# Performance work log

Hardware: AMD Instinct MI355X
Metric: run time of the kernel (lower is better)

The kernel has to match this reference:

```python
import jax
import jax.numpy as jnp
from jax import lax
import numpy as np

INPUT_DIM = 784
HIDDEN_DIM = 1024
BATCH = 256
N_BINS = 10


def setup_inputs() -> dict:
    key = jax.random.key(0)
    k1, k2, k3, k4, k5 = jax.random.split(key, 5)
    # kaiming-normal-ish init scales (faithful in spirit; exact values irrelevant for math)
    W = jax.random.normal(k1, (HIDDEN_DIM, INPUT_DIM), dtype=jnp.float32) * np.sqrt(2.0 / INPUT_DIM)
    c = jnp.zeros((HIDDEN_DIM, 1), dtype=jnp.float32)
    V = jax.random.normal(k2, (INPUT_DIM, HIDDEN_DIM, N_BINS), dtype=jnp.float32) * np.sqrt(2.0 / N_BINS)
    b = jnp.zeros((INPUT_DIM, N_BINS), dtype=jnp.float32)
    x = jax.random.randint(k3, (BATCH, INPUT_DIM), 0, N_BINS, dtype=jnp.int32)
    return {"x": x, "W": W, "c": c, "V": V, "b": b}


def reference(x, W, c, V, b):
    # x: [B, D] int pixel bins; W: [H, D]; c: [H, 1]; V: [D, H, 10]; b: [D, 10]
    B = x.shape[0]
    xf = x.astype(jnp.float32)  # [B, D]
    a0 = jnp.broadcast_to(c[:, 0][None, :], (B, W.shape[0]))  # [B, H]

    def step(a, inp):
        Vi, bi, Wi, xi = inp  # Vi:[H,10], bi:[10], Wi:[H], xi:[B]
        h = jax.nn.sigmoid(a)                       # [B, H]
        p = jax.nn.softmax(h @ Vi + bi, axis=1)     # [B, 10]
        a = a + xi[:, None] * Wi[None, :]           # rank-1 update, matches x_i @ W[:,i].T
        return a, p

    _, p_seq = lax.scan(step, a0, (V, b, W.T, xf.T))  # p_seq: [D, B, 10]
    p_hat = jnp.transpose(p_seq, (1, 2, 0))            # [B, 10, D] == torch.stack(p_hat, dim=2)
    return p_hat
```

## Files before the change

kernel.cpp:

```cpp
#include <hip/hip_runtime.h>
#include <stdint.h>

#define D_DIM 784
#define H_DIM 1024
#define B_DIM 256
#define NBIN  10
#define G_CH  8
#define T_CH  98
#define BT    16
#define BF    2
#define LOG2E 1.4426950408889634f

#define PSCAN_BLKS 512
#define VPREP_BLKS D_DIM
#define WPREP_BLKS 208

typedef _Float16 half8_t  __attribute__((ext_vector_type(8)));
typedef __fp16   fp16x2_t __attribute__((ext_vector_type(2)));
typedef float    float4_t __attribute__((ext_vector_type(4)));

__global__ void k_prep2(const float* __restrict__ W, const float* __restrict__ V,
                        const float* __restrict__ c, const int* __restrict__ x,
                        _Float16* __restrict__ Wt2h, _Float16* __restrict__ VB,
                        _Float16* __restrict__ PA) {
    __shared__ __align__(16) float smem[H_DIM * NBIN];
    int tid = threadIdx.x;
    int bx  = blockIdx.x;

    if (bx < PSCAN_BLKS) {
        int q  = bx;
        int b0 = (q & 127) * BF;
        int h  = (q >> 7) * 256 + tid;
        float* xs0 = smem;
        float* xs1 = smem + D_DIM;
        for (int qq = tid; qq < BF * (D_DIM / 4); qq += 256) {
            int bb = qq / (D_DIM / 4), r = qq % (D_DIM / 4);
            int4 xi = ((const int4*)(x + (size_t)(b0 + bb) * D_DIM))[r];
            float4 xf = make_float4((float)xi.x, (float)xi.y, (float)xi.z, (float)xi.w);
            *((float4*)((bb ? xs1 : xs0) + r * 4)) = xf;
        }
        float acc0 = c[h], acc1 = acc0;
        __syncthreads();
        const float4* w4 = (const float4*)(W + (size_t)h * D_DIM);
        _Float16* pa = PA + (size_t)b0 * H_DIM + h;

        auto pstore = [&](int t_) {
            pa[(size_t)t_ * (B_DIM * H_DIM)]         = (_Float16)(acc0 * LOG2E);
            pa[(size_t)t_ * (B_DIM * H_DIM) + H_DIM] = (_Float16)(acc1 * LOG2E);
        };
        auto pfma = [&](float4 w0_, float4 w1_, int t_) {
            float4 xa0 = *((const float4*)(xs0 + t_ * 8));
            float4 xa1 = *((const float4*)(xs0 + t_ * 8 + 4));
            float4 xb0 = *((const float4*)(xs1 + t_ * 8));
            float4 xb1 = *((const float4*)(xs1 + t_ * 8 + 4));
            acc0 += xa0.x*w0_.x + xa0.y*w0_.y + xa0.z*w0_.z + xa0.w*w0_.w
                  + xa1.x*w1_.x + xa1.y*w1_.y + xa1.z*w1_.z + xa1.w*w1_.w;
            acc1 += xb0.x*w0_.x + xb0.y*w0_.y + xb0.z*w0_.z + xb0.w*w0_.w
                  + xb1.x*w1_.x + xb1.y*w1_.y + xb1.z*w1_.z + xb1.w*w1_.w;
        };

        float4 wA0 = w4[0], wA1 = w4[1], wB0 = w4[2], wB1 = w4[3];
        for (int t = 0; t < T_CH - 2; t += 2) {
            float4 nA0 = w4[(t + 2) * 2], nA1 = w4[(t + 2) * 2 + 1];
            float4 nB0 = w4[(t + 3) * 2], nB1 = w4[(t + 3) * 2 + 1];
            pstore(t);     pfma(wA0, wA1, t);
            pstore(t + 1); pfma(wB0, wB1, t + 1);
            wA0 = nA0; wA1 = nA1; wB0 = nB0; wB1 = nB1;
        }
        pstore(96); pfma(wA0, wA1, 96);
        pstore(97);
    } else if (bx < PSCAN_BLKS + VPREP_BLKS) {
        int i = bx - PSCAN_BLKS;
        const float4* src = (const float4*)(V + (size_t)i * H_DIM * NBIN);
        #pragma unroll
        for (int qv = 0; qv < 10; ++qv) {
            float4 v = src[qv * 256 + tid];
            *((float4*)&smem[(qv * 256 + tid) * 4]) = v;
        }
        __syncthreads();
        #pragma unroll
        for (int qv = 0; qv < 8; ++qv) {
            int pair = qv * 256 + tid;
            int kk = pair >> 6, ll = pair & 63;
            int n = ll & 15, hb = kk * 32 + ((ll >> 4) & 3) * 8;
            union { _Float16 hh[8]; uint4 u; } o;
            #pragma unroll
            for (int jj = 0; jj < 8; ++jj)
                o.hh[jj] = (_Float16)((n < NBIN) ? smem[(hb + jj) * NBIN + n] : 0.0f);
            ((uint4*)VB)[(size_t)i * 2048 + pair] = o.u;
        }
    } else {
        int qw = bx - PSCAN_BLKS - VPREP_BLKS;
        int j0 = (qw % 13) * 64, h0 = (qw / 13) * 64;
        float (*t)[65] = (float(*)[65])smem;
        int tj = tid & 63, tr = tid >> 6;
        int j = j0 + tj;
        #pragma unroll
        for (int r = 0; r < 16; ++r) {
            int hh = tr * 16 + r;
            t[hh][tj] = (j < D_DIM) ? W[(size_t)(h0 + hh) * D_DIM + j] : 0.0f;
        }
        __syncthreads();
        #pragma unroll
        for (int r = 0; r < 16; ++r) {
            int jj = tr * 16 + r;
            int jo = j0 + jj;
            if (jo < D_DIM) Wt2h[(size_t)jo * H_DIM + h0 + tj] = (_Float16)(t[tj][jj] * LOG2E);
        }
    }
}

__global__ __launch_bounds__(256, 4)
void k_main(const _Float16* __restrict__ VB, const _Float16* __restrict__ Wt2h,
            const _Float16* __restrict__ PA, const int* __restrict__ x,
            const float* __restrict__ bias, float* __restrict__ out) {
    int bt  = blockIdx.x;
    int tc  = blockIdx.y;
    int tid = threadIdx.x;
    int w   = tid >> 6;
    int l   = tid & 63;
    int bl  = l & 15;
    int kg  = l >> 4;
    int bg  = bt * BT + bl;
    int i0  = tc * G_CH;

    __shared__ __align__(16) _Float16 wlds[G_CH][H_DIM];
    __shared__ float red[4][64][18];
    __shared__ float bs[G_CH][16];

    {
        int ii = tid >> 4, n = tid & 15;
        if (ii < G_CH) bs[ii][n] = (n < NBIN) ? bias[(size_t)(i0 + ii) * NBIN + n] : 0.0f;
    }
    {
        #pragma unroll
        for (int r = 0; r < G_CH; ++r) {
            uint2 v = ((const uint2*)(Wt2h + (size_t)(i0 + r) * H_DIM))[tid];
            *((uint2*)&wlds[r][tid * 4]) = v;
        }
    }
    float xvf[G_CH];
    {
        const int4* xp = (const int4*)(x + (size_t)bg * D_DIM + i0);
        int4 x0 = xp[0], x1 = xp[1];
        xvf[0] = (float)x0.x; xvf[1] = (float)x0.y; xvf[2] = (float)x0.z; xvf[3] = (float)x0.w;
        xvf[4] = (float)x1.x; xvf[5] = (float)x1.y; xvf[6] = (float)x1.z; xvf[7] = (float)x1.w;
    }
    float a[8][8];
    {
        const _Float16* src = PA + ((size_t)tc * B_DIM + bg) * H_DIM + w * 256 + kg * 8;
        #pragma unroll
        for (int m = 0; m < 8; ++m) {
            half8_t av = *((const half8_t*)(src + m * 32));
            #pragma unroll
            for (int j = 0; j < 8; ++j) a[m][j] = (float)av[j];
        }
    }

    const uint4* vp = (const uint4*)VB + ((size_t)i0 * 32 + w * 8) * 64 + l;
    uint4 vbuf[3];
    vbuf[0] = vp[0];
    vbuf[1] = vp[64];
    float4_t acc = {0.f, 0.f, 0.f, 0.f};

    auto step = [&](int mm) {
        const int ii = mm >> 3, m = mm & 7;
        if (mm + 2 < 64) {
            const int nn = mm + 2;
            vbuf[nn % 3] = vp[((nn >> 3) * 32 + (nn & 7)) * 64];
        }
        union { half8_t h8; uint u32[4]; } af;
        #pragma unroll
        for (int p = 0; p < 4; ++p) {
            float s0 = __builtin_amdgcn_rcpf(1.0f + __builtin_amdgcn_exp2f(-a[m][2 * p]));
            float s1 = __builtin_amdgcn_rcpf(1.0f + __builtin_amdgcn_exp2f(-a[m][2 * p + 1]));
            union { fp16x2_t v; uint u; } cv;
            cv.v = __builtin_amdgcn_cvt_pkrtz(s0, s1);
            af.u32[p] = cv.u;
        }
        union { half8_t h8; uint4 u; } bf;
        bf.u = vbuf[mm % 3];
        acc = __builtin_amdgcn_mfma_f32_16x16x32_f16(af.h8, bf.h8, acc, 0, 0, 0);
        half8_t wh = *((const half8_t*)&wlds[ii][w * 256 + kg * 8 + m * 32]);
        float xf = xvf[ii];
        a[m][0] += xf * (float)wh[0]; a[m][1] += xf * (float)wh[1];
        a[m][2] += xf * (float)wh[2]; a[m][3] += xf * (float)wh[3];
        a[m][4] += xf * (float)wh[4]; a[m][5] += xf * (float)wh[5];
        a[m][6] += xf * (float)wh[6]; a[m][7] += xf * (float)wh[7];
        if (m == 7) {
            int s = (ii & 3) * 4;
            red[w][l][s + 0] = acc[0]; red[w][l][s + 1] = acc[1];
            red[w][l][s + 2] = acc[2]; red[w][l][s + 3] = acc[3];
            acc = (float4_t){0.f, 0.f, 0.f, 0.f};
        }
    };

    auto softmax_store = [&](int half) {
        float p4[4];
        #pragma unroll
        for (int q = 0; q < 4; ++q) {
            int ii = half * 4 + q;
            float tot = red[0][l][q * 4 + w] + red[1][l][q * 4 + w]
                      + red[2][l][q * 4 + w] + red[3][l][q * 4 + w];
            float v = (bl < NBIN) ? tot + bs[ii][bl] : -3.0e38f;
            float vm = v;
            vm = fmaxf(vm, __shfl_xor(vm, 1));
            vm = fmaxf(vm, __shfl_xor(vm, 2));
            vm = fmaxf(vm, __shfl_xor(vm, 4));
            vm = fmaxf(vm, __shfl_xor(vm, 8));
            float e = __builtin_amdgcn_exp2f((v - vm) * LOG2E);
            float ss = e;
            ss += __shfl_xor(ss, 1); ss += __shfl_xor(ss, 2);
            ss += __shfl_xor(ss, 4); ss += __shfl_xor(ss, 8);
            p4[q] = e * __builtin_amdgcn_rcpf(ss);
        }
        if (bl < NBIN) {
            int b = bt * BT + kg * 4 + w;
            size_t base = ((size_t)b * NBIN + bl) * D_DIM + i0 + half * 4;
            float4 v = make_float4(p4[0], p4[1], p4[2], p4[3]);
            *((float4*)(out + base)) = v;
        }
    };

    __syncthreads();
    #pragma unroll
    for (int mm = 0; mm < 32; ++mm) step(mm);
    __syncthreads();
    softmax_store(0);
    __syncthreads();
    #pragma unroll
    for (int mm = 32; mm < 64; ++mm) step(mm);
    __syncthreads();
    softmax_store(1);
}

extern "C" void kernel_launch(void* const* d_in, const int* in_sizes, int n_in,
                              void* d_out, int out_size, void* d_ws, size_t ws_size,
                              hipStream_t stream) {
    const int*   x    = (const int*)d_in[0];
    const float* W    = (const float*)d_in[1];
    const float* c    = (const float*)d_in[2];
    const float* V    = (const float*)d_in[3];
    const float* bias = (const float*)d_in[4];
    float* out = (float*)d_out;

    char* ws = (char*)d_ws;
    size_t off = 0;
    _Float16* Wt2h = (_Float16*)(ws + off);
    off += (size_t)D_DIM * H_DIM * sizeof(_Float16);
    off = (off + 255) & ~(size_t)255;
    _Float16* VB = (_Float16*)(ws + off);
    off += (size_t)D_DIM * 32 * 64 * 8 * sizeof(_Float16);
    off = (off + 255) & ~(size_t)255;
    _Float16* PA = (_Float16*)(ws + off);

    k_prep2<<<dim3(PSCAN_BLKS + VPREP_BLKS + WPREP_BLKS), 256, 0, stream>>>(W, V, c, x, Wt2h, VB, PA);
    k_main<<<dim3(B_DIM / BT, T_CH), 256, 0, stream>>>(VB, Wt2h, PA, x, bias, out);
}
```

Before: 218.9 us.

## Halve prep LDS footprint and register-block prefix scan over two hidden units

The prefix-sum part of the prep kernel now has each thread handle two adjacent hidden units, which halves the number of scan blocks, reuses each shared x load across four accumulators, and writes packed half2 stores. The V-repack branch now processes its slice in two halves so shared memory shrinks from 40KB to 20KB, aiming for more resident blocks per CU. The cost is an extra barrier in the V path, more registers per thread in the scan, and fewer scan blocks to spread across the GPU.

```diff
diff --git a/kernel.cpp b/kernel.cpp
--- a/kernel.cpp
+++ b/kernel.cpp
@@ -11,7 +11,7 @@
 #define BF    2
 #define LOG2E 1.4426950408889634f
 
-#define PSCAN_BLKS 512
+#define PSCAN_BLKS 256
 #define VPREP_BLKS D_DIM
 #define WPREP_BLKS 208
 
@@ -23,14 +23,14 @@
                         const float* __restrict__ c, const int* __restrict__ x,
                         _Float16* __restrict__ Wt2h, _Float16* __restrict__ VB,
                         _Float16* __restrict__ PA) {
-    __shared__ __align__(16) float smem[H_DIM * NBIN];
+    __shared__ __align__(16) float smem[5120];
     int tid = threadIdx.x;
     int bx  = blockIdx.x;
 
     if (bx < PSCAN_BLKS) {
-        int q  = bx;
-        int b0 = (q & 127) * BF;
-        int h  = (q >> 7) * 256 + tid;
+        int b0 = (bx & 127) * BF;
+        int hg = bx >> 7;
+        int h0 = hg * 512 + tid * 2;
         float* xs0 = smem;
         float* xs1 = smem + D_DIM;
         for (int qq = tid; qq < BF * (D_DIM / 4); qq += 256) {
@@ -39,55 +39,69 @@
             float4 xf = make_float4((float)xi.x, (float)xi.y, (float)xi.z, (float)xi.w);
             *((float4*)((bb ? xs1 : xs0) + r * 4)) = xf;
         }
-        float acc0 = c[h], acc1 = acc0;
+        float c0 = c[h0], c1 = c[h0 + 1];
+        float acc00 = c0, acc01 = c1;
+        float acc10 = c0, acc11 = c1;
         __syncthreads();
-        const float4* w4 = (const float4*)(W + (size_t)h * D_DIM);
-        _Float16* pa = PA + (size_t)b0 * H_DIM + h;
+        const float4* w0 = (const float4*)(W + (size_t)h0 * D_DIM);
+        const float4* w1 = (const float4*)(W + (size_t)(h0 + 1) * D_DIM);
+        uint* pa0 = (uint*)PA + (size_t)b0 * (H_DIM / 2) + (h0 >> 1);
 
         auto pstore = [&](int t_) {
-            pa[(size_t)t_ * (B_DIM * H_DIM)]         = (_Float16)(acc0 * LOG2E);
-            pa[(size_t)t_ * (B_DIM * H_DIM) + H_DIM] = (_Float16)(acc1 * LOG2E);
+            union { _Float16 hh[2]; uint u; } u0, u1;
+            u0.hh[0] = (_Float16)(acc00 * LOG2E); u0.hh[1] = (_Float16)(acc01 * LOG2E);
+            u1.hh[0] = (_Float16)(acc10 * LOG2E); u1.hh[1] = (_Float16)(acc11 * LOG2E);
+            pa0[(size_t)t_ * (B_DIM * H_DIM / 2)] = u0.u;
+            pa0[(size_t)t_ * (B_DIM * H_DIM / 2) + (H_DIM / 2)] = u1.u;
         };
-        auto pfma = [&](float4 w0_, float4 w1_, int t_) {
-            float4 xa0 = *((const float4*)(xs0 + t_ * 8));
-            float4 xa1 = *((const float4*)(xs0 + t_ * 8 + 4));
-            float4 xb0 = *((const float4*)(xs1 + t_ * 8));
-            float4 xb1 = *((const float4*)(xs1 + t_ * 8 + 4));
-            acc0 += xa0.x*w0_.x + xa0.y*w0_.y + xa0.z*w0_.z + xa0.w*w0_.w
-                  + xa1.x*w1_.x + xa1.y*w1_.y + xa1.z*w1_.z + xa1.w*w1_.w;
-            acc1 += xb0.x*w0_.x + xb0.y*w0_.y + xb0.z*w0_.z + xb0.w*w0_.w
-                  + xb1.x*w1_.x + xb1.y*w1_.y + xb1.z*w1_.z + xb1.w*w1_.w;
+        auto pfma = [&](float4 a0_, float4 a1_, float4 b0_, float4 b1_, int t_) {
+            float4 x00 = *((const float4*)(xs0 + t_ * 8));
+            float4 x01 = *((const float4*)(xs0 + t_ * 8 + 4));
+            float4 x10 = *((const float4*)(xs1 + t_ * 8));
+            float4 x11 = *((const float4*)(xs1 + t_ * 8 + 4));
+            acc00 += x00.x*a0_.x + x00.y*a0_.y + x00.z*a0_.z + x00.w*a0_.w
+                   + x01.x*a1_.x + x01.y*a1_.y + x01.z*a1_.z + x01.w*a1_.w;
+            acc01 += x00.x*b0_.x + x00.y*b0_.y + x00.z*b0_.z + x00.w*b0_.w
+                   + x01.x*b1_.x + x01.y*b1_.y + x01.z*b1_.z + x01.w*b1_.w;
+            acc10 += x10.x*a0_.x + x10.y*a0_.y + x10.z*a0_.z + x10.w*a0_.w
+                   + x11.x*a1_.x + x11.y*a1_.y + x11.z*a1_.z + x11.w*a1_.w;
+            acc11 += x10.x*b0_.x + x10.y*b0_.y + x10.z*b0_.z + x10.w*b0_.w
+                   + x11.x*b1_.x + x11.y*b1_.y + x11.z*b1_.z + x11.w*b1_.w;
         };
 
-        float4 wA0 = w4[0], wA1 = w4[1], wB0 = w4[2], wB1 = w4[3];
-        for (int t = 0; t < T_CH - 2; t += 2) {
-            float4 nA0 = w4[(t + 2) * 2], nA1 = w4[(t + 2) * 2 + 1];
-            float4 nB0 = w4[(t + 3) * 2], nB1 = w4[(t + 3) * 2 + 1];
-            pstore(t);     pfma(wA0, wA1, t);
-            pstore(t + 1); pfma(wB0, wB1, t + 1);
-            wA0 = nA0; wA1 = nA1; wB0 = nB0; wB1 = nB1;
-        }
-        pstore(96); pfma(wA0, wA1, 96);
-        pstore(97);
+        float4 A0 = w0[0], A1 = w0[1], B0 = w1[0], B1 = w1[1];
+        for (int t = 0; t < T_CH; ++t) {
+            int tn = (t + 1 < T_CH) ? t + 1 : t;
+            float4 nA0 = w0[tn * 2], nA1 = w0[tn * 2 + 1];
+            float4 nB0 = w1[tn * 2], nB1 = w1[tn * 2 + 1];
+            pstore(t);
+            pfma(A0, A1, B0, B1, t);
+            A0 = nA0; A1 = nA1; B0 = nB0; B1 = nB1;
+        }
     } else if (bx < PSCAN_BLKS + VPREP_BLKS) {
         int i = bx - PSCAN_BLKS;
         const float4* src = (const float4*)(V + (size_t)i * H_DIM * NBIN);
-        #pragma unroll
-        for (int qv = 0; qv < 10; ++qv) {
-            float4 v = src[qv * 256 + tid];
-            *((float4*)&smem[(qv * 256 + tid) * 4]) = v;
-        }
-        __syncthreads();
-        #pragma unroll
-        for (int qv = 0; qv < 8; ++qv) {
-            int pair = qv * 256 + tid;
-            int kk = pair >> 6, ll = pair & 63;
-            int n = ll & 15, hb = kk * 32 + ((ll >> 4) & 3) * 8;
-            union { _Float16 hh[8]; uint4 u; } o;
+        uint4* dst = (uint4*)VB + (size_t)i * 2048;
+        #pragma unroll
+        for (int p = 0; p < 2; ++p) {
+            if (p) __syncthreads();
             #pragma unroll
-            for (int jj = 0; jj < 8; ++jj)
-                o.hh[jj] = (_Float16)((n < NBIN) ? smem[(hb + jj) * NBIN + n] : 0.0f);
-            ((uint4*)VB)[(size_t)i * 2048 + pair] = o.u;
+            for (int qv = 0; qv < 5; ++qv) {
+                float4 v = src[p * 1280 + qv * 256 + tid];
+                *((float4*)&smem[(qv * 256 + tid) * 4]) = v;
+            }
+            __syncthreads();
+            #pragma unroll
+            for (int qv = 0; qv < 4; ++qv) {
+                int pair = p * 1024 + qv * 256 + tid;
+                int kk = pair >> 6, ll = pair & 63;
+                int n = ll & 15, hb = kk * 32 + ((ll >> 4) & 3) * 8;
+                union { _Float16 hh[8]; uint4 u; } o;
+                #pragma unroll
+                for (int jj = 0; jj < 8; ++jj)
+                    o.hh[jj] = (_Float16)((n < NBIN) ? smem[(hb + jj) * NBIN + n - p * 5120] : 0.0f);
+                dst[pair] = o.u;
+            }
         }
     } else {
         int qw = bx - PSCAN_BLKS - VPREP_BLKS;
```

Measured after the change: 219.4 us. About the same (+0.3%).
